# Kernel optimization log

Hardware: AMD Instinct MI355X
Metric: run time of the kernel (lower is better)

## Reference

```python
import jax, jax.numpy as jnp
import numpy as np

HEADS = 8
LN_EPS = 1e-5


def _elu_plus_one(t):
    # F.elu(x) + 1 == exp(x) for x<0, x+1 for x>=0
    return jax.nn.elu(t) + 1.0


def setup_inputs() -> dict:
    key = jax.random.key(0)
    k1, k2, k3 = jax.random.split(key, 3)
    dim = 256
    x = jax.random.normal(k1, (16, dim, 64, 64), dtype=jnp.float32)
    w_qkv = jax.random.normal(k2, (3 * dim, dim), dtype=jnp.float32) * 0.02
    w_out = jax.random.normal(k3, (dim, dim), dtype=jnp.float32) * 0.02
    ln_gamma = jnp.ones((dim,), dtype=jnp.float32)
    ln_beta = jnp.zeros((dim,), dtype=jnp.float32)
    return {"x": x, "w_qkv": w_qkv, "w_out": w_out, "ln_gamma": ln_gamma, "ln_beta": ln_beta}


def reference(x, w_qkv, w_out, ln_gamma, ln_beta):
    b, c, h, w = x.shape
    hd = c // HEADS
    n = h * w
    # 1x1 conv == per-pixel matmul over channels
    qkv = jnp.einsum('bchw,oc->bohw', x, w_qkv)  # [b, 3c, h, w]
    q, k, v = jnp.split(qkv, 3, axis=1)
    q = q.reshape(b, HEADS, hd, n)
    k = k.reshape(b, HEADS, hd, n)
    v = v.reshape(b, HEADS, hd, n)
    qk = _elu_plus_one(q)
    kk = _elu_plus_one(k)
    # channel-wise kv reduction over spatial positions (NOT an outer product)
    kv = jnp.sum(kk * v, axis=-1, keepdims=True)        # [b, heads, hd, 1]
    denom = jnp.maximum(jnp.sum(kk, axis=-1, keepdims=True), 1e-6)
    out = qk * (kv / denom)                              # [b, heads, hd, n]
    out = out.reshape(b, c, h, w)
    out = jnp.einsum('bchw,oc->bohw', out, w_out)        # 1x1 output conv
    # LayerNorm over channel dim (module permutes to NHWC first)
    t = jnp.transpose(out, (0, 2, 3, 1))                 # [b, h, w, c]
    mu = jnp.mean(t, axis=-1, keepdims=True)
    var = jnp.mean(jnp.square(t - mu), axis=-1, keepdims=True)
    t = (t - mu) * jax.lax.rsqrt(var + LN_EPS) * ln_gamma + ln_beta
    return jnp.transpose(t, (0, 3, 1, 2))
```

## Files before the change

kernel.cpp:

```cpp
#include <hip/hip_runtime.h>


#define NB 16
#define NC 256
#define NN 4096
#define LN_EPS 1e-5f
#define IOSCALE (1.0f/1024.0f)

typedef _Float16 f16;
typedef _Float16 f16x8 __attribute__((ext_vector_type(8)));
typedef _Float16 f16x4v __attribute__((ext_vector_type(4)));
typedef float f32x4 __attribute__((ext_vector_type(4)));

typedef __attribute__((address_space(1))) const unsigned int* as1cu32;
typedef __attribute__((address_space(3))) unsigned int* as3u32;

__device__ __forceinline__ void gload16(const void* g, void* l) {
  __builtin_amdgcn_global_load_lds((as1cu32)g, (as3u32)l, 16, 0, 0);
}

__device__ __forceinline__ float elu1(float x) {
  return x > 0.f ? x + 1.f : __expf(x);
}

__device__ __forceinline__ int swz(int row, int unit) {
  return row * 64 + (((unit) ^ (row & 7)) << 3);
}

__global__ __launch_bounds__(256) void k_init(const float* __restrict__ w,
                                              f16* __restrict__ wh,
                                              float* __restrict__ kvden) {
  int i = blockIdx.x * 256 + threadIdx.x;
  if (i < 768 * 256) wh[i] = (f16)w[i];
  if (i < 8192) kvden[i] = 0.f;
}

__global__ __launch_bounds__(256) void k_transpose(const float* __restrict__ x,
                                                   f16* __restrict__ xh) {
  __shared__ float t[64 * 65];
  const int b = blockIdx.z, c0 = blockIdx.y * 64, n0 = blockIdx.x * 64;
  const int tid = threadIdx.x;
#pragma unroll
  for (int i = 0; i < 4; ++i) {
    int lin = tid + i * 256;
    int r = lin >> 4;
    int cg = lin & 15;
    const float4 v = *reinterpret_cast<const float4*>(
        &x[((size_t)(b * NC + c0 + r)) * NN + n0 + cg * 4]);
    t[r * 65 + cg * 4 + 0] = v.x;
    t[r * 65 + cg * 4 + 1] = v.y;
    t[r * 65 + cg * 4 + 2] = v.z;
    t[r * 65 + cg * 4 + 3] = v.w;
  }
  __syncthreads();
#pragma unroll
  for (int i = 0; i < 4; ++i) {
    int lin = tid + i * 256;
    int nr = lin >> 4;
    int cg = lin & 15;
    f16x4v h;
    h[0] = (f16)t[(cg * 4 + 0) * 65 + nr];
    h[1] = (f16)t[(cg * 4 + 1) * 65 + nr];
    h[2] = (f16)t[(cg * 4 + 2) * 65 + nr];
    h[3] = (f16)t[(cg * 4 + 3) * 65 + nr];
    *reinterpret_cast<f16x4v*>(&xh[((size_t)(b * NN + n0 + nr)) * NC + c0 + cg * 4]) = h;
  }
}

__global__ __launch_bounds__(256) void k_gemm_q(const f16* __restrict__ xh,
                                                const f16* __restrict__ wh,
                                                f16* __restrict__ qh) {
  __shared__ __align__(16) f16 At[128 * 64];
  __shared__ __align__(16) f16 Bt[128 * 64];
  const int b = blockIdx.z;
  const int n0 = blockIdx.x * 128;
  const int o0 = blockIdx.y * 128;
  const int tid = threadIdx.x;
  const int lane = tid & 63;
  const int wv = tid >> 6;
  const int wn = wv >> 1, wo = wv & 1;
  const int l15 = lane & 15, lg = lane >> 4;
  const int srow = lane >> 3;
  const int ssrc = ((lane & 7) ^ srow) * 8;

  f32x4 acc[4][4] = {};

  for (int ks = 0; ks < 4; ++ks) {
    const int c0 = ks * 64;
#pragma unroll
    for (int it = 0; it < 4; ++it) {
      const int seg = wv * 4 + it;
      const int row = seg * 8 + srow;
      gload16(xh + ((size_t)(b * NN + n0 + row)) * NC + c0 + ssrc, At + seg * 512);
      gload16(wh + (size_t)(o0 + row) * NC + c0 + ssrc, Bt + seg * 512);
    }
    __syncthreads();
#pragma unroll
    for (int kk = 0; kk < 2; ++kk) {
      const int ku = kk * 4 + lg;
      f16x8 af[4], bf[4];
#pragma unroll
      for (int m = 0; m < 4; ++m)
        af[m] = *(const f16x8*)(At + swz(wn * 64 + m * 16 + l15, ku));
#pragma unroll
      for (int n = 0; n < 4; ++n)
        bf[n] = *(const f16x8*)(Bt + swz(wo * 64 + n * 16 + l15, ku));
#pragma unroll
      for (int m = 0; m < 4; ++m)
#pragma unroll
        for (int n = 0; n < 4; ++n)
          acc[m][n] = __builtin_amdgcn_mfma_f32_16x16x32_f16(af[m], bf[n], acc[m][n], 0, 0, 0);
    }
    __syncthreads();
  }
#pragma unroll
  for (int m = 0; m < 4; ++m) {
    const int nr = n0 + wn * 64 + m * 16 + lg * 4;
#pragma unroll
    for (int n = 0; n < 4; ++n) {
      const int oc = o0 + wo * 64 + n * 16 + l15;
#pragma unroll
      for (int j = 0; j < 4; ++j)
        qh[((size_t)(b * NN + nr + j)) * NC + oc] = (f16)elu1(acc[m][n][j]);
    }
  }
}

__global__ __launch_bounds__(256) void k_gemm_kv(const f16* __restrict__ xh,
                                                 const f16* __restrict__ wh,
                                                 float* __restrict__ kv,
                                                 float* __restrict__ den) {
  __shared__ __align__(16) f16 At[128 * 64];
  __shared__ __align__(16) f16 Bt[128 * 64];
  const int b = blockIdx.z;
  const int n0 = blockIdx.x * 128;
  const int cc0 = blockIdx.y * 64;
  const int tid = threadIdx.x;
  const int lane = tid & 63;
  const int wv = tid >> 6;
  const int l15 = lane & 15, lg = lane >> 4;
  const int srow = lane >> 3;
  const int ssrc = ((lane & 7) ^ srow) * 8;

  f32x4 acc[2][8] = {};

  for (int ks = 0; ks < 4; ++ks) {
    const int c0 = ks * 64;
#pragma unroll
    for (int it = 0; it < 4; ++it) {
      const int seg = wv * 4 + it;
      const int row = seg * 8 + srow;
      gload16(xh + ((size_t)(b * NN + n0 + row)) * NC + c0 + ssrc, At + seg * 512);
      const int wrow = row < 64 ? 256 + cc0 + row : 512 + cc0 + (row - 64);
      gload16(wh + (size_t)wrow * NC + c0 + ssrc, Bt + seg * 512);
    }
    __syncthreads();
#pragma unroll
    for (int kk = 0; kk < 2; ++kk) {
      const int ku = kk * 4 + lg;
      f16x8 af[2], bf[8];
#pragma unroll
      for (int m = 0; m < 2; ++m)
        af[m] = *(const f16x8*)(At + swz(wv * 32 + m * 16 + l15, ku));
#pragma unroll
      for (int f = 0; f < 8; ++f)
        bf[f] = *(const f16x8*)(Bt + swz(f * 16 + l15, ku));
#pragma unroll
      for (int m = 0; m < 2; ++m)
#pragma unroll
        for (int f = 0; f < 8; ++f)
          acc[m][f] = __builtin_amdgcn_mfma_f32_16x16x32_f16(af[m], bf[f], acc[m][f], 0, 0, 0);
    }
    __syncthreads();
  }
  float pkv[4] = {0.f, 0.f, 0.f, 0.f}, pden[4] = {0.f, 0.f, 0.f, 0.f};
#pragma unroll
  for (int f = 0; f < 4; ++f)
#pragma unroll
    for (int m = 0; m < 2; ++m)
#pragma unroll
      for (int j = 0; j < 4; ++j) {
        const float kk = elu1(acc[m][f][j]);
        pkv[f] += kk * acc[m][f + 4][j];
        pden[f] += kk;
      }
#pragma unroll
  for (int f = 0; f < 4; ++f) {
    pkv[f] += __shfl_xor(pkv[f], 16, 64);
    pkv[f] += __shfl_xor(pkv[f], 32, 64);
    pden[f] += __shfl_xor(pden[f], 16, 64);
    pden[f] += __shfl_xor(pden[f], 32, 64);
  }
  if (lane < 16) {
#pragma unroll
    for (int f = 0; f < 4; ++f) {
      const int c = cc0 + f * 16 + lane;
      atomicAdd(&kv[b * NC + c], pkv[f]);
      atomicAdd(&den[b * NC + c], pden[f]);
    }
  }
}

__global__ __launch_bounds__(256) void k_ws(const float* __restrict__ wout,
                                            const float* __restrict__ kv,
                                            const float* __restrict__ den,
                                            f16* __restrict__ wsc) {
  int i = blockIdx.x * 256 + threadIdx.x;
  int c = i & 255;
  int o = (i >> 8) & 255;
  int b = i >> 16;
  float s = kv[b * 256 + c] / fmaxf(den[b * 256 + c], 1e-6f);
  wsc[i] = (f16)(wout[o * 256 + c] * s * 1024.0f);
}

__global__ __launch_bounds__(256) void k_gemm2_ln(const f16* __restrict__ wsc,
                                                  const f16* __restrict__ qh,
                                                  const float* __restrict__ gamma,
                                                  const float* __restrict__ beta,
                                                  float* __restrict__ out) {
  __shared__ __align__(16) f16 At[256 * 64];
  __shared__ __align__(16) f16 Bt[64 * 64];
  __shared__ float red1[4][64];
  __shared__ float red2[4][64];
  __shared__ float smu[64], srs[64];
  const int b = blockIdx.y;
  const int n0 = blockIdx.x * 64;
  const int tid = threadIdx.x;
  const int lane = tid & 63;
  const int wv = tid >> 6;
  const int l15 = lane & 15, lg = lane >> 4;
  const int srow = lane >> 3;
  const int ssrc = ((lane & 7) ^ srow) * 8;
  const f16* wsb = wsc + (size_t)b * NC * NC;

  f32x4 acc[4][4] = {};

  for (int ks = 0; ks < 4; ++ks) {
    const int c0 = ks * 64;
#pragma unroll
    for (int it = 0; it < 8; ++it) {
      const int seg = wv * 8 + it;
      const int row = seg * 8 + srow;
      gload16(wsb + (size_t)row * NC + c0 + ssrc, At + seg * 512);
    }
#pragma unroll
    for (int it = 0; it < 2; ++it) {
      const int seg = wv * 2 + it;
      const int row = seg * 8 + srow;
      gload16(qh + ((size_t)(b * NN + n0 + row)) * NC + c0 + ssrc, Bt + seg * 512);
    }
    __syncthreads();
#pragma unroll
    for (int kk = 0; kk < 2; ++kk) {
      const int ku = kk * 4 + lg;
      f16x8 af[4], bf[4];
#pragma unroll
      for (int m = 0; m < 4; ++m)
        af[m] = *(const f16x8*)(At + swz(wv * 64 + m * 16 + l15, ku));
#pragma unroll
      for (int f = 0; f < 4; ++f)
        bf[f] = *(const f16x8*)(Bt + swz(f * 16 + l15, ku));
#pragma unroll
      for (int m = 0; m < 4; ++m)
#pragma unroll
        for (int f = 0; f < 4; ++f)
          acc[m][f] = __builtin_amdgcn_mfma_f32_16x16x32_f16(af[m], bf[f], acc[m][f], 0, 0, 0);
    }
    __syncthreads();
  }
  float s1[4] = {0, 0, 0, 0}, s2[4] = {0, 0, 0, 0};
#pragma unroll
  for (int f = 0; f < 4; ++f)
#pragma unroll
    for (int m = 0; m < 4; ++m)
#pragma unroll
      for (int j = 0; j < 4; ++j) {
        const float v = acc[m][f][j];
        s1[f] += v;
        s2[f] += v * v;
      }
#pragma unroll
  for (int f = 0; f < 4; ++f) {
    s1[f] += __shfl_xor(s1[f], 16, 64);
    s1[f] += __shfl_xor(s1[f], 32, 64);
    s2[f] += __shfl_xor(s2[f], 16, 64);
    s2[f] += __shfl_xor(s2[f], 32, 64);
  }
  if (lane < 16) {
#pragma unroll
    for (int f = 0; f < 4; ++f) {
      red1[wv][f * 16 + lane] = s1[f];
      red2[wv][f * 16 + lane] = s2[f];
    }
  }
  __syncthreads();
  if (tid < 64) {
    const float a1 = red1[0][tid] + red1[1][tid] + red1[2][tid] + red1[3][tid];
    const float a2 = red2[0][tid] + red2[1][tid] + red2[2][tid] + red2[3][tid];
    const float mu = a1 * (IOSCALE / 256.f);
    const float e2 = a2 * (IOSCALE * IOSCALE / 256.f);
    smu[tid] = mu;
    srs[tid] = rsqrtf(e2 - mu * mu + LN_EPS);
  }
  __syncthreads();
#pragma unroll
  for (int m = 0; m < 4; ++m) {
    const int ob = wv * 64 + m * 16 + lg * 4;
#pragma unroll
    for (int j = 0; j < 4; ++j) {
      const int o = ob + j;
      const float g = gamma[o], be = beta[o];
#pragma unroll
      for (int f = 0; f < 4; ++f) {
        const int col = f * 16 + l15;
        const float v = acc[m][f][j] * IOSCALE;
        out[((size_t)(b * NC + o)) * NN + n0 + col] = (v - smu[col]) * srs[col] * g + be;
      }
    }
  }
}

extern "C" void kernel_launch(void* const* d_in, const int* in_sizes, int n_in,
                              void* d_out, int out_size, void* d_ws, size_t ws_size,
                              hipStream_t stream) {
  const float* x = (const float*)d_in[0];
  const float* w_qkv = (const float*)d_in[1];
  const float* w_out = (const float*)d_in[2];
  const float* ln_g = (const float*)d_in[3];
  const float* ln_b = (const float*)d_in[4];
  float* out = (float*)d_out;

  char* wsb = (char*)d_ws;
  const size_t OFF_WH = 0;
  const size_t OFF_XH = OFF_WH + 393216;
  const size_t OFF_QH = OFF_XH + 33554432;
  const size_t OFF_KV = OFF_QH + 33554432;
  const size_t OFF_DEN = OFF_KV + 16384;
  const size_t OFF_WSC = OFF_DEN + 16384;

  f16* wh = (f16*)(wsb + OFF_WH);
  f16* xh = (f16*)(wsb + OFF_XH);
  f16* qh = (f16*)(wsb + OFF_QH);
  float* kv = (float*)(wsb + OFF_KV);
  float* den = (float*)(wsb + OFF_DEN);
  f16* wsc = (f16*)(wsb + OFF_WSC);

  k_init<<<768, 256, 0, stream>>>(w_qkv, wh, kv);
  k_transpose<<<dim3(64, 4, 16), 256, 0, stream>>>(x, xh);
  k_gemm_q<<<dim3(32, 2, 16), 256, 0, stream>>>(xh, wh, qh);
  k_gemm_kv<<<dim3(32, 4, 16), 256, 0, stream>>>(xh, wh, kv, den);
  k_ws<<<4096, 256, 0, stream>>>(w_out, kv, den, wsc);
  k_gemm2_ln<<<dim3(64, 16), 256, 0, stream>>>(wsc, qh, ln_g, ln_b, out);
}
```

Before: 95.79 us.

## Fuse Q projection into output GEMM+LayerNorm, apply kv scale in-register

Drops the separate Q GEMM kernel and its 32MB f16 qh round-trip. Q is now recomputed inside the final kernel, has ELU and the per-channel kv/den scale applied, and is staged in shared memory before multiplying by an f16 copy of w_out. This also removes the per-batch scaled-weight kernel (k_ws). The kv kernel is restructured into 512-thread blocks that compute all 256 channels of K then V per 64-pixel tile, with the trade-off of more LDS per block and serialized K/V phases.

```diff
diff --git a/kernel.cpp b/kernel.cpp
--- a/kernel.cpp
+++ b/kernel.cpp
@@ -27,11 +27,14 @@
   return row * 64 + (((unit) ^ (row & 7)) << 3);
 }
 
-__global__ __launch_bounds__(256) void k_init(const float* __restrict__ w,
+__global__ __launch_bounds__(256) void k_init(const float* __restrict__ wqkv,
+                                              const float* __restrict__ wout,
                                               f16* __restrict__ wh,
+                                              f16* __restrict__ wouth,
                                               float* __restrict__ kvden) {
   int i = blockIdx.x * 256 + threadIdx.x;
-  if (i < 768 * 256) wh[i] = (f16)w[i];
+  wh[i] = (f16)wqkv[i];
+  if (i < 65536) wouth[i] = (f16)wout[i];
   if (i < 8192) kvden[i] = 0.f;
 }
 
@@ -67,111 +70,75 @@
   }
 }
 
-__global__ __launch_bounds__(256) void k_gemm_q(const f16* __restrict__ xh,
-                                                const f16* __restrict__ wh,
-                                                f16* __restrict__ qh) {
-  __shared__ __align__(16) f16 At[128 * 64];
-  __shared__ __align__(16) f16 Bt[128 * 64];
-  const int b = blockIdx.z;
-  const int n0 = blockIdx.x * 128;
-  const int o0 = blockIdx.y * 128;
+__global__ __launch_bounds__(512) void k_kv(const f16* __restrict__ xh,
+                                            const f16* __restrict__ wh,
+                                            float* __restrict__ kv,
+                                            float* __restrict__ den) {
+  __shared__ __align__(16) f16 Xt[64 * 64];
+  __shared__ __align__(16) f16 Bt[256 * 64];
+  const int b = blockIdx.y;
+  const int n0 = blockIdx.x * 64;
   const int tid = threadIdx.x;
   const int lane = tid & 63;
   const int wv = tid >> 6;
-  const int wn = wv >> 1, wo = wv & 1;
+  const int ng = wv >> 2;
+  const int cg = wv & 3;
   const int l15 = lane & 15, lg = lane >> 4;
-  const int srow = lane >> 3;
-  const int ssrc = ((lane & 7) ^ srow) * 8;
-
-  f32x4 acc[4][4] = {};
+  const int lr = lane >> 3;
+  const int ssrc = ((lane & 7) ^ lr) * 8;
+
+  f32x4 kacc[2][4] = {};
+  f32x4 vacc[2][4] = {};
 
   for (int ks = 0; ks < 4; ++ks) {
     const int c0 = ks * 64;
+    __syncthreads();
+    gload16(xh + ((size_t)(b * NN + n0 + wv * 8 + lr)) * NC + c0 + ssrc, Xt + wv * 512);
 #pragma unroll
     for (int it = 0; it < 4; ++it) {
       const int seg = wv * 4 + it;
-      const int row = seg * 8 + srow;
-      gload16(xh + ((size_t)(b * NN + n0 + row)) * NC + c0 + ssrc, At + seg * 512);
-      gload16(wh + (size_t)(o0 + row) * NC + c0 + ssrc, Bt + seg * 512);
+      gload16(wh + (size_t)(256 + seg * 8 + lr) * NC + c0 + ssrc, Bt + seg * 512);
     }
     __syncthreads();
 #pragma unroll
     for (int kk = 0; kk < 2; ++kk) {
       const int ku = kk * 4 + lg;
-      f16x8 af[4], bf[4];
-#pragma unroll
-      for (int m = 0; m < 4; ++m)
-        af[m] = *(const f16x8*)(At + swz(wn * 64 + m * 16 + l15, ku));
-#pragma unroll
-      for (int n = 0; n < 4; ++n)
-        bf[n] = *(const f16x8*)(Bt + swz(wo * 64 + n * 16 + l15, ku));
-#pragma unroll
-      for (int m = 0; m < 4; ++m)
-#pragma unroll
-        for (int n = 0; n < 4; ++n)
-          acc[m][n] = __builtin_amdgcn_mfma_f32_16x16x32_f16(af[m], bf[n], acc[m][n], 0, 0, 0);
-    }
-    __syncthreads();
-  }
-#pragma unroll
-  for (int m = 0; m < 4; ++m) {
-    const int nr = n0 + wn * 64 + m * 16 + lg * 4;
-#pragma unroll
-    for (int n = 0; n < 4; ++n) {
-      const int oc = o0 + wo * 64 + n * 16 + l15;
-#pragma unroll
-      for (int j = 0; j < 4; ++j)
-        qh[((size_t)(b * NN + nr + j)) * NC + oc] = (f16)elu1(acc[m][n][j]);
-    }
-  }
-}
-
-__global__ __launch_bounds__(256) void k_gemm_kv(const f16* __restrict__ xh,
-                                                 const f16* __restrict__ wh,
-                                                 float* __restrict__ kv,
-                                                 float* __restrict__ den) {
-  __shared__ __align__(16) f16 At[128 * 64];
-  __shared__ __align__(16) f16 Bt[128 * 64];
-  const int b = blockIdx.z;
-  const int n0 = blockIdx.x * 128;
-  const int cc0 = blockIdx.y * 64;
-  const int tid = threadIdx.x;
-  const int lane = tid & 63;
-  const int wv = tid >> 6;
-  const int l15 = lane & 15, lg = lane >> 4;
-  const int srow = lane >> 3;
-  const int ssrc = ((lane & 7) ^ srow) * 8;
-
-  f32x4 acc[2][8] = {};
-
-  for (int ks = 0; ks < 4; ++ks) {
-    const int c0 = ks * 64;
+      f16x8 af[2], bf[4];
+#pragma unroll
+      for (int m = 0; m < 2; ++m)
+        af[m] = *(const f16x8*)(Xt + swz(ng * 32 + m * 16 + l15, ku));
+#pragma unroll
+      for (int f = 0; f < 4; ++f)
+        bf[f] = *(const f16x8*)(Bt + swz(cg * 64 + f * 16 + l15, ku));
+#pragma unroll
+      for (int m = 0; m < 2; ++m)
+#pragma unroll
+        for (int f = 0; f < 4; ++f)
+          kacc[m][f] = __builtin_amdgcn_mfma_f32_16x16x32_f16(af[m], bf[f], kacc[m][f], 0, 0, 0);
+    }
+    __syncthreads();
 #pragma unroll
     for (int it = 0; it < 4; ++it) {
       const int seg = wv * 4 + it;
-      const int row = seg * 8 + srow;
-      gload16(xh + ((size_t)(b * NN + n0 + row)) * NC + c0 + ssrc, At + seg * 512);
-      const int wrow = row < 64 ? 256 + cc0 + row : 512 + cc0 + (row - 64);
-      gload16(wh + (size_t)wrow * NC + c0 + ssrc, Bt + seg * 512);
+      gload16(wh + (size_t)(512 + seg * 8 + lr) * NC + c0 + ssrc, Bt + seg * 512);
     }
     __syncthreads();
 #pragma unroll
     for (int kk = 0; kk < 2; ++kk) {
       const int ku = kk * 4 + lg;
-      f16x8 af[2], bf[8];
+      f16x8 af[2], bf[4];
 #pragma unroll
       for (int m = 0; m < 2; ++m)
-        af[m] = *(const f16x8*)(At + swz(wv * 32 + m * 16 + l15, ku));
-#pragma unroll
-      for (int f = 0; f < 8; ++f)
-        bf[f] = *(const f16x8*)(Bt + swz(f * 16 + l15, ku));
+        af[m] = *(const f16x8*)(Xt + swz(ng * 32 + m * 16 + l15, ku));
+#pragma unroll
+      for (int f = 0; f < 4; ++f)
+        bf[f] = *(const f16x8*)(Bt + swz(cg * 64 + f * 16 + l15, ku));
 #pragma unroll
       for (int m = 0; m < 2; ++m)
 #pragma unroll
-        for (int f = 0; f < 8; ++f)
-          acc[m][f] = __builtin_amdgcn_mfma_f32_16x16x32_f16(af[m], bf[f], acc[m][f], 0, 0, 0);
-    }
-    __syncthreads();
+        for (int f = 0; f < 4; ++f)
+          vacc[m][f] = __builtin_amdgcn_mfma_f32_16x16x32_f16(af[m], bf[f], vacc[m][f], 0, 0, 0);
+    }
   }
   float pkv[4] = {0.f, 0.f, 0.f, 0.f}, pden[4] = {0.f, 0.f, 0.f, 0.f};
 #pragma unroll
@@ -180,8 +147,8 @@
     for (int m = 0; m < 2; ++m)
 #pragma unroll
       for (int j = 0; j < 4; ++j) {
-        const float kk = elu1(acc[m][f][j]);
-        pkv[f] += kk * acc[m][f + 4][j];
+        const float kk = elu1(kacc[m][f][j]);
+        pkv[f] += kk * vacc[m][f][j];
         pden[f] += kk;
       }
 #pragma unroll
@@ -194,34 +161,26 @@
   if (lane < 16) {
 #pragma unroll
     for (int f = 0; f < 4; ++f) {
-      const int c = cc0 + f * 16 + lane;
+      const int c = cg * 64 + f * 16 + lane;
       atomicAdd(&kv[b * NC + c], pkv[f]);
       atomicAdd(&den[b * NC + c], pden[f]);
     }
   }
 }
 
-__global__ __launch_bounds__(256) void k_ws(const float* __restrict__ wout,
-                                            const float* __restrict__ kv,
-                                            const float* __restrict__ den,
-                                            f16* __restrict__ wsc) {
-  int i = blockIdx.x * 256 + threadIdx.x;
-  int c = i & 255;
-  int o = (i >> 8) & 255;
-  int b = i >> 16;
-  float s = kv[b * 256 + c] / fmaxf(den[b * 256 + c], 1e-6f);
-  wsc[i] = (f16)(wout[o * 256 + c] * s * 1024.0f);
-}
-
-__global__ __launch_bounds__(256) void k_gemm2_ln(const f16* __restrict__ wsc,
-                                                  const f16* __restrict__ qh,
-                                                  const float* __restrict__ gamma,
-                                                  const float* __restrict__ beta,
-                                                  float* __restrict__ out) {
-  __shared__ __align__(16) f16 At[256 * 64];
-  __shared__ __align__(16) f16 Bt[64 * 64];
-  __shared__ float red1[4][64];
-  __shared__ float red2[4][64];
+__global__ __launch_bounds__(256) void k_fused2(const f16* __restrict__ xh,
+                                                const f16* __restrict__ wh,
+                                                const f16* __restrict__ wouth,
+                                                const float* __restrict__ kv,
+                                                const float* __restrict__ den,
+                                                const float* __restrict__ gamma,
+                                                const float* __restrict__ beta,
+                                                float* __restrict__ out) {
+  __shared__ __align__(16) f16 Xt[64 * 64];
+  __shared__ __align__(16) f16 Wt[256 * 64];
+  __shared__ __align__(16) f16 Q[64 * 264];
+  __shared__ float s1024[256];
+  __shared__ float red1[4][64], red2[4][64];
   __shared__ float smu[64], srs[64];
   const int b = blockIdx.y;
   const int n0 = blockIdx.x * 64;
@@ -229,25 +188,25 @@
   const int lane = tid & 63;
   const int wv = tid >> 6;
   const int l15 = lane & 15, lg = lane >> 4;
-  const int srow = lane >> 3;
-  const int ssrc = ((lane & 7) ^ srow) * 8;
-  const f16* wsb = wsc + (size_t)b * NC * NC;
+  const int lr = lane >> 3;
+  const int ssrc = ((lane & 7) ^ lr) * 8;
+
+  s1024[tid] = kv[b * NC + tid] / fmaxf(den[b * NC + tid], 1e-6f) * 1024.0f;
 
   f32x4 acc[4][4] = {};
 
   for (int ks = 0; ks < 4; ++ks) {
     const int c0 = ks * 64;
+    __syncthreads();
+#pragma unroll
+    for (int it = 0; it < 2; ++it) {
+      const int seg = wv * 2 + it;
+      gload16(xh + ((size_t)(b * NN + n0 + seg * 8 + lr)) * NC + c0 + ssrc, Xt + seg * 512);
+    }
 #pragma unroll
     for (int it = 0; it < 8; ++it) {
       const int seg = wv * 8 + it;
-      const int row = seg * 8 + srow;
-      gload16(wsb + (size_t)row * NC + c0 + ssrc, At + seg * 512);
-    }
-#pragma unroll
-    for (int it = 0; it < 2; ++it) {
-      const int seg = wv * 2 + it;
-      const int row = seg * 8 + srow;
-      gload16(qh + ((size_t)(b * NN + n0 + row)) * NC + c0 + ssrc, Bt + seg * 512);
+      gload16(wh + (size_t)(seg * 8 + lr) * NC + c0 + ssrc, Wt + seg * 512);
     }
     __syncthreads();
 #pragma unroll
@@ -256,18 +215,61 @@
       f16x8 af[4], bf[4];
 #pragma unroll
       for (int m = 0; m < 4; ++m)
-        af[m] = *(const f16x8*)(At + swz(wv * 64 + m * 16 + l15, ku));
+        af[m] = *(const f16x8*)(Wt + swz(wv * 64 + m * 16 + l15, ku));
 #pragma unroll
       for (int f = 0; f < 4; ++f)
-        bf[f] = *(const f16x8*)(Bt + swz(f * 16 + l15, ku));
+        bf[f] = *(const f16x8*)(Xt + swz(f * 16 + l15, ku));
 #pragma unroll
       for (int m = 0; m < 4; ++m)
 #pragma unroll
         for (int f = 0; f < 4; ++f)
           acc[m][f] = __builtin_amdgcn_mfma_f32_16x16x32_f16(af[m], bf[f], acc[m][f], 0, 0, 0);
     }
-    __syncthreads();
-  }
+  }
+
+#pragma unroll
+  for (int m = 0; m < 4; ++m) {
+    const int cq = wv * 64 + m * 16 + lg * 4;
+#pragma unroll
+    for (int f = 0; f < 4; ++f) {
+      const int n = f * 16 + l15;
+      f16x4v h;
+#pragma unroll
+      for (int j = 0; j < 4; ++j)
+        h[j] = (f16)(elu1(acc[m][f][j]) * s1024[cq + j]);
+      *reinterpret_cast<f16x4v*>(Q + n * 264 + cq) = h;
+    }
+  }
+
+  f32x4 acc2[4][4] = {};
+  for (int ks = 0; ks < 4; ++ks) {
+    const int c0 = ks * 64;
+    __syncthreads();
+#pragma unroll
+    for (int it = 0; it < 8; ++it) {
+      const int seg = wv * 8 + it;
+      gload16(wouth + (size_t)(seg * 8 + lr) * NC + c0 + ssrc, Wt + seg * 512);
+    }
+    __syncthreads();
+#pragma unroll
+    for (int kk = 0; kk < 2; ++kk) {
+      const int ku = kk * 4 + lg;
+      const int kb = c0 + kk * 32 + lg * 8;
+      f16x8 af[4], bf[4];
+#pragma unroll
+      for (int m = 0; m < 4; ++m)
+        af[m] = *(const f16x8*)(Wt + swz(wv * 64 + m * 16 + l15, ku));
+#pragma unroll
+      for (int f = 0; f < 4; ++f)
+        bf[f] = *(const f16x8*)(Q + (f * 16 + l15) * 264 + kb);
+#pragma unroll
+      for (int m = 0; m < 4; ++m)
+#pragma unroll
+        for (int f = 0; f < 4; ++f)
+          acc2[m][f] = __builtin_amdgcn_mfma_f32_16x16x32_f16(af[m], bf[f], acc2[m][f], 0, 0, 0);
+    }
+  }
+
   float s1[4] = {0, 0, 0, 0}, s2[4] = {0, 0, 0, 0};
 #pragma unroll
   for (int f = 0; f < 4; ++f)
@@ -275,7 +277,7 @@
     for (int m = 0; m < 4; ++m)
 #pragma unroll
       for (int j = 0; j < 4; ++j) {
-        const float v = acc[m][f][j];
+        const float v = acc2[m][f][j];
         s1[f] += v;
         s2[f] += v * v;
       }
@@ -313,7 +315,7 @@
 #pragma unroll
       for (int f = 0; f < 4; ++f) {
         const int col = f * 16 + l15;
-        const float v = acc[m][f][j] * IOSCALE;
+        const float v = acc2[m][f][j] * IOSCALE;
         out[((size_t)(b * NC + o)) * NN + n0 + col] = (v - smu[col]) * srs[col] * g + be;
       }
     }
@@ -332,23 +334,19 @@
 
   char* wsb = (char*)d_ws;
   const size_t OFF_WH = 0;
-  const size_t OFF_XH = OFF_WH + 393216;
-  const size_t OFF_QH = OFF_XH + 33554432;
-  const size_t OFF_KV = OFF_QH + 33554432;
+  const size_t OFF_WOUTH = 393216;
+  const size_t OFF_XH = OFF_WOUTH + 131072;
+  const size_t OFF_KV = OFF_XH + 33554432;
   const size_t OFF_DEN = OFF_KV + 16384;
-  const size_t OFF_WSC = OFF_DEN + 16384;
 
   f16* wh = (f16*)(wsb + OFF_WH);
+  f16* wouth = (f16*)(wsb + OFF_WOUTH);
   f16* xh = (f16*)(wsb + OFF_XH);
-  f16* qh = (f16*)(wsb + OFF_QH);
   float* kv = (float*)(wsb + OFF_KV);
   float* den = (float*)(wsb + OFF_DEN);
-  f16* wsc = (f16*)(wsb + OFF_WSC);
-
-  k_init<<<768, 256, 0, stream>>>(w_qkv, wh, kv);
+
+  k_init<<<768, 256, 0, stream>>>(w_qkv, w_out, wh, wouth, kv);
   k_transpose<<<dim3(64, 4, 16), 256, 0, stream>>>(x, xh);
-  k_gemm_q<<<dim3(32, 2, 16), 256, 0, stream>>>(xh, wh, qh);
-  k_gemm_kv<<<dim3(32, 4, 16), 256, 0, stream>>>(xh, wh, kv, den);
-  k_ws<<<4096, 256, 0, stream>>>(w_out, kv, den, wsc);
-  k_gemm2_ln<<<dim3(64, 16), 256, 0, stream>>>(wsc, qh, ln_g, ln_b, out);
-}
+  k_kv<<<dim3(64, 16), 512, 0, stream>>>(xh, wh, kv, den);
+  k_fused2<<<dim3(64, 16), 256, 0, stream>>>(xh, wh, wouth, kv, den, ln_g, ln_b, out);
+}
```

New measurement: 84.87 us. -11.4%, faster.
